# Kernel optimization log

Measured on AMD Instinct MI355X. Metric: run time of the kernel, lower is better.

The kernel has to match this reference:

```python
import jax, jax.numpy as jnp
import numpy as np

B, IN, OUT = 1024, 512, 512

def setup_inputs() -> dict:
    key = jax.random.key(0)
    k1, k2 = jax.random.split(key)
    X = jax.random.normal(k1, (B, IN), dtype=jnp.float32)
    # init_std=0.02 path in the torch module: normal(std=0.02)
    W = jax.random.normal(k2, (OUT, IN), dtype=jnp.float32) * 0.02
    return {"X": X, "W": W}

def reference(X, W):
    # Tropical (min-plus) matmul: out[b, j] = min_i (X[b, i] + W[j, i])
    # Broadcast-add produces [B, OUT, IN]; min-reduce over IN.
    return jnp.min(X[:, None, :] + W[None, :, :], axis=-1)
```

## Files before the change

kernel.cpp:

```cpp
#include <hip/hip_runtime.h>
#include <math.h>


#define B_DIM   1024
#define IN_DIM  512
#define OUT_DIM 512

__global__ __launch_bounds__(256)
void MinPlus_wt4_pack(const float* __restrict__ W, float4* __restrict__ WT4) {
    __shared__ float Ls[64][68];
    const int tid = threadIdx.x;
    const int j0 = blockIdx.x * 64;
    const int k0 = blockIdx.y * 64;

#pragma unroll
    for (int r = 0; r < 4; ++r) {
        const int jj = (tid >> 4) + r * 16;
        const int kq = tid & 15;
        const float4 v = *reinterpret_cast<const float4*>(&W[(j0 + jj) * IN_DIM + k0 + 4 * kq]);
        *reinterpret_cast<float4*>(&Ls[jj][4 * kq]) = v;
    }
    __syncthreads();

    const int jj  = tid & 63;
    const int k4b = tid >> 6;
#pragma unroll
    for (int r = 0; r < 4; ++r) {
        const int k4l = r * 4 + k4b;
        const float4 v = *reinterpret_cast<const float4*>(&Ls[jj][4 * k4l]);
        WT4[(size_t)(blockIdx.y * 16 + k4l) * OUT_DIM + j0 + jj] = v;
    }
}

__global__ __launch_bounds__(1024)
void MinPlus_70832600646269_kernel(const float* __restrict__ X,
                                   const float4* __restrict__ WT4,
                                   float* __restrict__ out)
{
    __shared__ float Xs[4][IN_DIM];
    __shared__ float part[16][4][256];

    const int tid  = threadIdx.x;
    const int lane = tid & 63;
    const int wid  = tid >> 6;
    const int j0   = blockIdx.x * 256;
    const int b0   = blockIdx.y * 4;

    if (tid < 512)
        reinterpret_cast<float4*>(&Xs[0][0])[tid] =
            reinterpret_cast<const float4*>(X + (size_t)b0 * IN_DIM)[tid];
    __syncthreads();

    float acc[4][4];
#pragma unroll
    for (int b = 0; b < 4; ++b)
#pragma unroll
        for (int jq = 0; jq < 4; ++jq) acc[b][jq] = INFINITY;

#pragma unroll
    for (int c = 0; c < 2; ++c) {
        float4 w[4][4];
#pragma unroll
        for (int q = 0; q < 4; ++q)
#pragma unroll
            for (int jq = 0; jq < 4; ++jq)
                w[q][jq] = WT4[(size_t)(wid * 8 + c * 4 + q) * OUT_DIM + j0 + jq * 64 + lane];

#pragma unroll
        for (int b = 0; b < 4; ++b) {
            const float4* __restrict__ xrow =
                reinterpret_cast<const float4*>(&Xs[b][wid * 32 + c * 16]);
#pragma unroll
            for (int q = 0; q < 4; ++q) {
                const float4 x = xrow[q];
#pragma unroll
                for (int jq = 0; jq < 4; ++jq) {
                    const float4 u = w[q][jq];
                    acc[b][jq] = fminf(fminf(acc[b][jq], u.x + x.x), u.y + x.y);
                    acc[b][jq] = fminf(fminf(acc[b][jq], u.z + x.z), u.w + x.w);
                }
            }
        }
    }

#pragma unroll
    for (int b = 0; b < 4; ++b)
#pragma unroll
        for (int jq = 0; jq < 4; ++jq)
            part[wid][b][jq * 64 + lane] = acc[b][jq];

    __syncthreads();

    {
        const int b  = tid >> 8;
        const int jj = tid & 255;
        float m = part[0][b][jj];
#pragma unroll
        for (int p = 1; p < 16; ++p) m = fminf(m, part[p][b][jj]);
        out[(size_t)(b0 + b) * OUT_DIM + j0 + jj] = m;
    }
}

extern "C" void kernel_launch(void* const* d_in, const int* in_sizes, int n_in,
                              void* d_out, int out_size, void* d_ws, size_t ws_size,
                              hipStream_t stream) {
    const float* X = (const float*)d_in[0];
    const float* W = (const float*)d_in[1];
    float* out = (float*)d_out;
    float4* WT4 = (float4*)d_ws;

    MinPlus_wt4_pack<<<dim3(OUT_DIM / 64, IN_DIM / 64), 256, 0, stream>>>(W, WT4);

    MinPlus_70832600646269_kernel<<<dim3(OUT_DIM / 256, B_DIM / 4), 1024, 0, stream>>>(X, WT4, out);
}
```

Measured before the change: 26.22 us.

## Double batch rows per block, software-pipeline W loads, vectorize final reduction

Each block now handles 8 batch rows instead of 4, so every W element loaded into registers is reused across twice as many rows and the grid is halved. W loads are split into four stages with double-buffered registers, prefetching the next stage while the current one computes, and the first W load is issued before the barrier that waits on the X copy. The cross-wave reduction now reads and writes float4 values using half the threads. Shared memory rises to about 144KB per block, which may limit occupancy to one block per CU.

```diff
diff --git a/kernel.cpp b/kernel.cpp
--- a/kernel.cpp
+++ b/kernel.cpp
@@ -37,45 +37,54 @@
                                    const float4* __restrict__ WT4,
                                    float* __restrict__ out)
 {
-    __shared__ float Xs[4][IN_DIM];
-    __shared__ float part[16][4][256];
+    __shared__ float Xs[8][IN_DIM];
+    __shared__ float part[16][8][256];
 
     const int tid  = threadIdx.x;
     const int lane = tid & 63;
     const int wid  = tid >> 6;
     const int j0   = blockIdx.x * 256;
-    const int b0   = blockIdx.y * 4;
+    const int b0   = blockIdx.y * 8;
 
-    if (tid < 512)
-        reinterpret_cast<float4*>(&Xs[0][0])[tid] =
-            reinterpret_cast<const float4*>(X + (size_t)b0 * IN_DIM)[tid];
-    __syncthreads();
+    reinterpret_cast<float4*>(&Xs[0][0])[tid] =
+        reinterpret_cast<const float4*>(X + (size_t)b0 * IN_DIM)[tid];
 
-    float acc[4][4];
+    float acc[8][4];
 #pragma unroll
-    for (int b = 0; b < 4; ++b)
+    for (int b = 0; b < 8; ++b)
 #pragma unroll
         for (int jq = 0; jq < 4; ++jq) acc[b][jq] = INFINITY;
 
+    float4 w[2][2][4];
 #pragma unroll
-    for (int c = 0; c < 2; ++c) {
-        float4 w[4][4];
+    for (int q2 = 0; q2 < 2; ++q2)
 #pragma unroll
-        for (int q = 0; q < 4; ++q)
-#pragma unroll
-            for (int jq = 0; jq < 4; ++jq)
-                w[q][jq] = WT4[(size_t)(wid * 8 + c * 4 + q) * OUT_DIM + j0 + jq * 64 + lane];
+        for (int jq = 0; jq < 4; ++jq)
+            w[0][q2][jq] = WT4[(size_t)(wid * 8 + q2) * OUT_DIM + j0 + jq * 64 + lane];
+
+    __syncthreads();
 
 #pragma unroll
-        for (int b = 0; b < 4; ++b) {
-            const float4* __restrict__ xrow =
-                reinterpret_cast<const float4*>(&Xs[b][wid * 32 + c * 16]);
+    for (int qt = 0; qt < 4; ++qt) {
+        const int cur = qt & 1, nxt = cur ^ 1;
+        if (qt < 3) {
 #pragma unroll
-            for (int q = 0; q < 4; ++q) {
-                const float4 x = xrow[q];
+            for (int q2 = 0; q2 < 2; ++q2)
+#pragma unroll
+                for (int jq = 0; jq < 4; ++jq)
+                    w[nxt][q2][jq] =
+                        WT4[(size_t)(wid * 8 + (qt + 1) * 2 + q2) * OUT_DIM + j0 + jq * 64 + lane];
+        }
+#pragma unroll
+        for (int b = 0; b < 8; ++b) {
+            const float4* __restrict__ xq =
+                reinterpret_cast<const float4*>(&Xs[b][wid * 32 + qt * 8]);
+#pragma unroll
+            for (int q2 = 0; q2 < 2; ++q2) {
+                const float4 x = xq[q2];
 #pragma unroll
                 for (int jq = 0; jq < 4; ++jq) {
-                    const float4 u = w[q][jq];
+                    const float4 u = w[cur][q2][jq];
                     acc[b][jq] = fminf(fminf(acc[b][jq], u.x + x.x), u.y + x.y);
                     acc[b][jq] = fminf(fminf(acc[b][jq], u.z + x.z), u.w + x.w);
                 }
@@ -84,20 +93,26 @@
     }
 
 #pragma unroll
-    for (int b = 0; b < 4; ++b)
+    for (int b = 0; b < 8; ++b)
 #pragma unroll
         for (int jq = 0; jq < 4; ++jq)
             part[wid][b][jq * 64 + lane] = acc[b][jq];
 
     __syncthreads();
 
-    {
-        const int b  = tid >> 8;
-        const int jj = tid & 255;
-        float m = part[0][b][jj];
+    if (tid < 512) {
+        const int b  = tid >> 6;
+        const int j4 = (tid & 63) * 4;
+        float4 m = *reinterpret_cast<const float4*>(&part[0][b][j4]);
 #pragma unroll
-        for (int p = 1; p < 16; ++p) m = fminf(m, part[p][b][jj]);
-        out[(size_t)(b0 + b) * OUT_DIM + j0 + jj] = m;
+        for (int p = 1; p < 16; ++p) {
+            const float4 v = *reinterpret_cast<const float4*>(&part[p][b][j4]);
+            m.x = fminf(m.x, v.x);
+            m.y = fminf(m.y, v.y);
+            m.z = fminf(m.z, v.z);
+            m.w = fminf(m.w, v.w);
+        }
+        *reinterpret_cast<float4*>(&out[(size_t)(b0 + b) * OUT_DIM + j0 + j4]) = m;
     }
 }
 
@@ -111,5 +126,5 @@
 
     MinPlus_wt4_pack<<<dim3(OUT_DIM / 64, IN_DIM / 64), 256, 0, stream>>>(W, WT4);
 
-    MinPlus_70832600646269_kernel<<<dim3(OUT_DIM / 256, B_DIM / 4), 1024, 0, stream>>>(X, WT4, out);
+    MinPlus_70832600646269_kernel<<<dim3(OUT_DIM / 256, B_DIM / 8), 1024, 0, stream>>>(X, WT4, out);
 }
```

After: 21.86 us. 16.6% less time.

## Process eight batch rows per block, feeding four through scalar loads

Applied to the files above, without the earlier changes.

Each block now covers 8 batch rows instead of 4. Four rows come from the LDS as before, and the other four are fetched into scalar registers with inline s_load_dwordx16, so X reads for them are shared across the wavefront. This halves the grid and the number of W tile reloads from global memory, and doubles arithmetic per loaded W value. The partial-min buffer is repacked as float4 for the final reduction. The inline asm with manual waitcnt and the higher SGPR/VGPR pressure may hurt occupancy.

```diff
diff --git a/kernel.cpp b/kernel.cpp
--- a/kernel.cpp
+++ b/kernel.cpp
@@ -5,6 +5,8 @@
 #define B_DIM   1024
 #define IN_DIM  512
 #define OUT_DIM 512
+
+typedef float f16v __attribute__((ext_vector_type(16)));
 
 __global__ __launch_bounds__(256)
 void MinPlus_wt4_pack(const float* __restrict__ W, float4* __restrict__ WT4) {
@@ -37,67 +39,119 @@
                                    const float4* __restrict__ WT4,
                                    float* __restrict__ out)
 {
-    __shared__ float Xs[4][IN_DIM];
-    __shared__ float part[16][4][256];
+    __shared__ float  Xs[4][IN_DIM];
+    __shared__ float4 part[16][8][64];
 
     const int tid  = threadIdx.x;
     const int lane = tid & 63;
     const int wid  = tid >> 6;
     const int j0   = blockIdx.x * 256;
-    const int b0   = blockIdx.y * 4;
+    const int b0   = blockIdx.y * 8;
 
     if (tid < 512)
         reinterpret_cast<float4*>(&Xs[0][0])[tid] =
             reinterpret_cast<const float4*>(X + (size_t)b0 * IN_DIM)[tid];
-    __syncthreads();
 
-    float acc[4][4];
+    const uint64_t xaddr = (uint64_t)(X + (size_t)(b0 + 4) * IN_DIM + wid * 32);
+    const uint32_t xlo = __builtin_amdgcn_readfirstlane((uint32_t)xaddr);
+    const uint32_t xhi = __builtin_amdgcn_readfirstlane((uint32_t)(xaddr >> 32));
+    const uint64_t sbase = ((uint64_t)xhi << 32) | xlo;
+
+    const float4* __restrict__ wbase = WT4 + j0 + lane;
+    const int g0 = wid * 8;
+
+    float accL[4][4], accS[4][4];
 #pragma unroll
     for (int b = 0; b < 4; ++b)
 #pragma unroll
-        for (int jq = 0; jq < 4; ++jq) acc[b][jq] = INFINITY;
+        for (int jq = 0; jq < 4; ++jq) { accL[b][jq] = INFINITY; accS[b][jq] = INFINITY; }
+
+    f16v s0, s1, s2, s3;
+
+    __syncthreads();
 
 #pragma unroll
-    for (int c = 0; c < 2; ++c) {
+    for (int h = 0; h < 2; ++h) {
+        if (h == 0) {
+            asm volatile("s_load_dwordx16 %0, %4, 0x0\n\t"
+                         "s_load_dwordx16 %1, %4, 0x800\n\t"
+                         "s_load_dwordx16 %2, %4, 0x1000\n\t"
+                         "s_load_dwordx16 %3, %4, 0x1800"
+                         : "=&s"(s0), "=&s"(s1), "=&s"(s2), "=&s"(s3) : "s"(sbase));
+        } else {
+            asm volatile("s_load_dwordx16 %0, %4, 0x40\n\t"
+                         "s_load_dwordx16 %1, %4, 0x840\n\t"
+                         "s_load_dwordx16 %2, %4, 0x1040\n\t"
+                         "s_load_dwordx16 %3, %4, 0x1840"
+                         : "=&s"(s0), "=&s"(s1), "=&s"(s2), "=&s"(s3) : "s"(sbase));
+        }
+
         float4 w[4][4];
 #pragma unroll
         for (int q = 0; q < 4; ++q)
 #pragma unroll
             for (int jq = 0; jq < 4; ++jq)
-                w[q][jq] = WT4[(size_t)(wid * 8 + c * 4 + q) * OUT_DIM + j0 + jq * 64 + lane];
+                w[q][jq] = wbase[(size_t)(g0 + h * 4 + q) * OUT_DIM + jq * 64];
 
 #pragma unroll
         for (int b = 0; b < 4; ++b) {
-            const float4* __restrict__ xrow =
-                reinterpret_cast<const float4*>(&Xs[b][wid * 32 + c * 16]);
 #pragma unroll
             for (int q = 0; q < 4; ++q) {
-                const float4 x = xrow[q];
+                const float4 x = *reinterpret_cast<const float4*>(
+                    &Xs[b][wid * 32 + h * 16 + q * 4]);
 #pragma unroll
                 for (int jq = 0; jq < 4; ++jq) {
                     const float4 u = w[q][jq];
-                    acc[b][jq] = fminf(fminf(acc[b][jq], u.x + x.x), u.y + x.y);
-                    acc[b][jq] = fminf(fminf(acc[b][jq], u.z + x.z), u.w + x.w);
+                    accL[b][jq] = fminf(fminf(accL[b][jq], u.x + x.x), u.y + x.y);
+                    accL[b][jq] = fminf(fminf(accL[b][jq], u.z + x.z), u.w + x.w);
                 }
+            }
+        }
+
+        asm volatile("s_waitcnt lgkmcnt(0)" : "+s"(s0), "+s"(s1), "+s"(s2), "+s"(s3));
+
+#pragma unroll
+        for (int q = 0; q < 4; ++q) {
+#pragma unroll
+            for (int jq = 0; jq < 4; ++jq) {
+                const float4 u = w[q][jq];
+                accS[0][jq] = fminf(fminf(accS[0][jq], u.x + s0[4*q+0]), u.y + s0[4*q+1]);
+                accS[0][jq] = fminf(fminf(accS[0][jq], u.z + s0[4*q+2]), u.w + s0[4*q+3]);
+                accS[1][jq] = fminf(fminf(accS[1][jq], u.x + s1[4*q+0]), u.y + s1[4*q+1]);
+                accS[1][jq] = fminf(fminf(accS[1][jq], u.z + s1[4*q+2]), u.w + s1[4*q+3]);
+                accS[2][jq] = fminf(fminf(accS[2][jq], u.x + s2[4*q+0]), u.y + s2[4*q+1]);
+                accS[2][jq] = fminf(fminf(accS[2][jq], u.z + s2[4*q+2]), u.w + s2[4*q+3]);
+                accS[3][jq] = fminf(fminf(accS[3][jq], u.x + s3[4*q+0]), u.y + s3[4*q+1]);
+                accS[3][jq] = fminf(fminf(accS[3][jq], u.z + s3[4*q+2]), u.w + s3[4*q+3]);
             }
         }
     }
 
 #pragma unroll
-    for (int b = 0; b < 4; ++b)
-#pragma unroll
-        for (int jq = 0; jq < 4; ++jq)
-            part[wid][b][jq * 64 + lane] = acc[b][jq];
+    for (int b = 0; b < 4; ++b) {
+        part[wid][b][lane]     = make_float4(accL[b][0], accL[b][1], accL[b][2], accL[b][3]);
+        part[wid][b + 4][lane] = make_float4(accS[b][0], accS[b][1], accS[b][2], accS[b][3]);
+    }
 
     __syncthreads();
 
-    {
-        const int b  = tid >> 8;
-        const int jj = tid & 255;
-        float m = part[0][b][jj];
+    if (tid < 512) {
+        const int b = tid >> 6;
+        const int l = tid & 63;
+        float4 m = part[0][b][l];
 #pragma unroll
-        for (int p = 1; p < 16; ++p) m = fminf(m, part[p][b][jj]);
-        out[(size_t)(b0 + b) * OUT_DIM + j0 + jj] = m;
+        for (int p = 1; p < 16; ++p) {
+            const float4 v = part[p][b][l];
+            m.x = fminf(m.x, v.x);
+            m.y = fminf(m.y, v.y);
+            m.z = fminf(m.z, v.z);
+            m.w = fminf(m.w, v.w);
+        }
+        float* orow = out + (size_t)(b0 + b) * OUT_DIM + j0;
+        orow[l]       = m.x;
+        orow[64 + l]  = m.y;
+        orow[128 + l] = m.z;
+        orow[192 + l] = m.w;
     }
 }
 
@@ -111,5 +165,5 @@
 
     MinPlus_wt4_pack<<<dim3(OUT_DIM / 64, IN_DIM / 64), 256, 0, stream>>>(W, WT4);
 
-    MinPlus_70832600646269_kernel<<<dim3(OUT_DIM / 256, B_DIM / 4), 1024, 0, stream>>>(X, WT4, out);
+    MinPlus_70832600646269_kernel<<<dim3(OUT_DIM / 256, B_DIM / 8), 1024, 0, stream>>>(X, WT4, out);
 }
```

After: 21.96 us. 1.19x faster.

## Drop W transpose kernel; reduce along K lanes with shuffle tree and packed adds

Applied to the files above, without the earlier changes.

Removes the separate W-transpose pre-pass and the LDS staging of X. Each wave now loads row-major X and W directly, with lanes split across the K dimension, and computes a 4x8 output tile using v_pk_add_f32. The K partials are then combined with a butterfly shuffle transpose-reduce instead of an LDS partial buffer and block barriers. This saves a kernel launch and shared-memory traffic, but each thread reuses fewer operands from registers, so there is more global/L2 load traffic per output and more shuffle work.

```diff
diff --git a/kernel.cpp b/kernel.cpp
--- a/kernel.cpp
+++ b/kernel.cpp
@@ -6,98 +6,102 @@
 #define IN_DIM  512
 #define OUT_DIM 512
 
-__global__ __launch_bounds__(256)
-void MinPlus_wt4_pack(const float* __restrict__ W, float4* __restrict__ WT4) {
-    __shared__ float Ls[64][68];
-    const int tid = threadIdx.x;
-    const int j0 = blockIdx.x * 64;
-    const int k0 = blockIdx.y * 64;
+typedef float v2f __attribute__((ext_vector_type(2)));
 
-#pragma unroll
-    for (int r = 0; r < 4; ++r) {
-        const int jj = (tid >> 4) + r * 16;
-        const int kq = tid & 15;
-        const float4 v = *reinterpret_cast<const float4*>(&W[(j0 + jj) * IN_DIM + k0 + 4 * kq]);
-        *reinterpret_cast<float4*>(&Ls[jj][4 * kq]) = v;
-    }
-    __syncthreads();
+__device__ __forceinline__ v2f mk2(float a, float b) { v2f r; r.x = a; r.y = b; return r; }
 
-    const int jj  = tid & 63;
-    const int k4b = tid >> 6;
-#pragma unroll
-    for (int r = 0; r < 4; ++r) {
-        const int k4l = r * 4 + k4b;
-        const float4 v = *reinterpret_cast<const float4*>(&Ls[jj][4 * k4l]);
-        WT4[(size_t)(blockIdx.y * 16 + k4l) * OUT_DIM + j0 + jj] = v;
-    }
+__device__ __forceinline__ v2f pk_add(v2f a, v2f b) {
+    v2f d;
+    asm("v_pk_add_f32 %0, %1, %2" : "=v"(d) : "v"(a), "v"(b));
+    return d;
 }
 
-__global__ __launch_bounds__(1024)
+__global__ __launch_bounds__(512)
 void MinPlus_70832600646269_kernel(const float* __restrict__ X,
-                                   const float4* __restrict__ WT4,
+                                   const float* __restrict__ W,
                                    float* __restrict__ out)
 {
-    __shared__ float Xs[4][IN_DIM];
-    __shared__ float part[16][4][256];
-
     const int tid  = threadIdx.x;
     const int lane = tid & 63;
     const int wid  = tid >> 6;
-    const int j0   = blockIdx.x * 256;
-    const int b0   = blockIdx.y * 4;
+    const int jp   = lane >> 5;
+    const int kg   = lane & 31;
 
-    if (tid < 512)
-        reinterpret_cast<float4*>(&Xs[0][0])[tid] =
-            reinterpret_cast<const float4*>(X + (size_t)b0 * IN_DIM)[tid];
-    __syncthreads();
+    const int jb = blockIdx.x * 16 + (wid >> 2) * 8;
+    const int bb = blockIdx.y * 16 + (wid & 3) * 4;
 
     float acc[4][4];
 #pragma unroll
     for (int b = 0; b < 4; ++b)
 #pragma unroll
-        for (int jq = 0; jq < 4; ++jq) acc[b][jq] = INFINITY;
+        for (int jt = 0; jt < 4; ++jt) acc[b][jt] = INFINITY;
+
+    const float* __restrict__ xp = X + (size_t)bb * IN_DIM + kg * 4;
+    const float* __restrict__ wp = W + (size_t)(jb + jp) * IN_DIM + kg * 4;
 
 #pragma unroll
-    for (int c = 0; c < 2; ++c) {
-        float4 w[4][4];
+    for (int s = 0; s < 4; ++s) {
+        float4 x4[4], w4[4];
 #pragma unroll
-        for (int q = 0; q < 4; ++q)
+        for (int b = 0; b < 4; ++b)
+            x4[b] = *reinterpret_cast<const float4*>(xp + (size_t)b * IN_DIM + s * 128);
 #pragma unroll
-            for (int jq = 0; jq < 4; ++jq)
-                w[q][jq] = WT4[(size_t)(wid * 8 + c * 4 + q) * OUT_DIM + j0 + jq * 64 + lane];
+        for (int jt = 0; jt < 4; ++jt)
+            w4[jt] = *reinterpret_cast<const float4*>(wp + (size_t)(jt * 2) * IN_DIM + s * 128);
 
 #pragma unroll
         for (int b = 0; b < 4; ++b) {
-            const float4* __restrict__ xrow =
-                reinterpret_cast<const float4*>(&Xs[b][wid * 32 + c * 16]);
+            const v2f xlo = mk2(x4[b].x, x4[b].y);
+            const v2f xhi = mk2(x4[b].z, x4[b].w);
 #pragma unroll
-            for (int q = 0; q < 4; ++q) {
-                const float4 x = xrow[q];
-#pragma unroll
-                for (int jq = 0; jq < 4; ++jq) {
-                    const float4 u = w[q][jq];
-                    acc[b][jq] = fminf(fminf(acc[b][jq], u.x + x.x), u.y + x.y);
-                    acc[b][jq] = fminf(fminf(acc[b][jq], u.z + x.z), u.w + x.w);
-                }
+            for (int jt = 0; jt < 4; ++jt) {
+                const v2f t0 = pk_add(mk2(w4[jt].x, w4[jt].y), xlo);
+                const v2f t1 = pk_add(mk2(w4[jt].z, w4[jt].w), xhi);
+                acc[b][jt] = fminf(fminf(acc[b][jt], t0.x), t0.y);
+                acc[b][jt] = fminf(fminf(acc[b][jt], t1.x), t1.y);
             }
         }
     }
 
+    float A[16];
 #pragma unroll
-    for (int b = 0; b < 4; ++b)
+    for (int m = 0; m < 16; ++m) A[m] = acc[m >> 2][m & 3];
+
+    float B[8];
 #pragma unroll
-        for (int jq = 0; jq < 4; ++jq)
-            part[wid][b][jq * 64 + lane] = acc[b][jq];
+    for (int p = 0; p < 8; ++p) {
+        const float t = fminf(A[2 * p],     __shfl_xor(A[2 * p],     16));
+        const float u = fminf(A[2 * p + 1], __shfl_xor(A[2 * p + 1], 16));
+        B[p] = (lane & 16) ? u : t;
+    }
+    float C[4];
+#pragma unroll
+    for (int p = 0; p < 4; ++p) {
+        const float t = fminf(B[2 * p],     __shfl_xor(B[2 * p],     8));
+        const float u = fminf(B[2 * p + 1], __shfl_xor(B[2 * p + 1], 8));
+        C[p] = (lane & 8) ? u : t;
+    }
+    float D[2];
+#pragma unroll
+    for (int p = 0; p < 2; ++p) {
+        const float t = fminf(C[2 * p],     __shfl_xor(C[2 * p],     4));
+        const float u = fminf(C[2 * p + 1], __shfl_xor(C[2 * p + 1], 4));
+        D[p] = (lane & 4) ? u : t;
+    }
+    float E;
+    {
+        const float t = fminf(D[0], __shfl_xor(D[0], 2));
+        const float u = fminf(D[1], __shfl_xor(D[1], 2));
+        E = (lane & 2) ? u : t;
+    }
+    E = fminf(E, __shfl_xor(E, 1));
 
-    __syncthreads();
-
-    {
-        const int b  = tid >> 8;
-        const int jj = tid & 255;
-        float m = part[0][b][jj];
-#pragma unroll
-        for (int p = 1; p < 16; ++p) m = fminf(m, part[p][b][jj]);
-        out[(size_t)(b0 + b) * OUT_DIM + j0 + jj] = m;
+    const int m = ((kg >> 4) & 1) | (((kg >> 3) & 1) << 1)
+                | (((kg >> 2) & 1) << 2) | (((kg >> 1) & 1) << 3);
+    if (!(lane & 1)) {
+        const int b_loc = m >> 2;
+        const int jt    = m & 3;
+        out[(size_t)(bb + b_loc) * OUT_DIM + jb + jt * 2 + jp] = E;
     }
 }
 
@@ -107,9 +111,7 @@
     const float* X = (const float*)d_in[0];
     const float* W = (const float*)d_in[1];
     float* out = (float*)d_out;
-    float4* WT4 = (float4*)d_ws;
 
-    MinPlus_wt4_pack<<<dim3(OUT_DIM / 64, IN_DIM / 64), 256, 0, stream>>>(W, WT4);
-
-    MinPlus_70832600646269_kernel<<<dim3(OUT_DIM / 256, B_DIM / 4), 1024, 0, stream>>>(X, WT4, out);
+    dim3 grid(OUT_DIM / 16, B_DIM / 16);
+    MinPlus_70832600646269_kernel<<<grid, 512, 0, stream>>>(X, W, out);
 }
```

Measured after the change: 25.41 us. 1.03x faster.
